# Optimization experiments

Hardware: AMD Instinct MI355X
Metric: run time of the kernel (lower is better)

The kernel has to match this reference:

```python
import jax, jax.numpy as jnp
import numpy as np

EMB_DIM, TREE_DIM, OUT_DIM, VOCAB = 256, 256, 3, 10000
T, B, LEVELS = 255, 128, 8  # complete binary tree of depth 8, 128 trees per input


def _build_forest():
    # node j = T-1-heap(j): root (heap 0) is the LAST node so stack_last_h picks the root.
    heap = np.arange(T)
    depth = np.floor(np.log2(heap + 1)).astype(np.int64)  # 0..7
    node_order = np.empty(T, dtype=np.int64)
    node_order[T - 1 - heap] = (LEVELS - 1) - depth       # leaves=0, root=7
    internal = np.arange((T - 1) // 2)                     # heaps with two children
    parent = np.repeat(T - 1 - internal, 2)
    child = np.stack([T - 1 - (2 * internal + 1), T - 1 - (2 * internal + 2)], 1).reshape(-1)
    edges = np.stack([parent, child], axis=1)              # (254, 2)
    edge_order = node_order[parent]
    offs = (np.arange(B) * T)[:, None, None]
    adj = (edges[None] + offs).reshape(-1, 2)              # (B*254, 2)
    return np.tile(node_order, B), adj, np.tile(edge_order, B)


def setup_inputs() -> dict:
    key = jax.random.key(0)
    ks = jax.random.split(key, 16)
    no, adj, eo = _build_forest()
    D = TREE_DIM
    s_e = 1.0 / np.sqrt(EMB_DIM)
    s_t = 1.0 / np.sqrt(D)
    return {
        'feat_cube': jax.random.randint(ks[0], (B * T,), 0, VOCAB),
        'feat_a': jax.random.randint(ks[1], (B * T,), 0, VOCAB),
        'feat_b': jax.random.randint(ks[2], (B * T,), 0, VOCAB),
        'node_order': jnp.asarray(no),
        'adjacency_list': jnp.asarray(adj),
        'edge_order': jnp.asarray(eo),
        'num_levels': LEVELS,
        'num_trees': B,
        'emb': jax.random.normal(ks[3], (VOCAB, EMB_DIM), jnp.float32),
        'W_iou': jax.random.normal(ks[4], (3 * D, EMB_DIM), jnp.float32) * s_e,
        'b_iou': jnp.zeros((3 * D,), jnp.float32),
        'U_iou': jax.random.normal(ks[5], (3 * D, D), jnp.float32) * s_t,
        'W_f': jax.random.normal(ks[6], (D, EMB_DIM), jnp.float32) * s_e,
        'b_f': jnp.zeros((D,), jnp.float32),
        'U_f': jax.random.normal(ks[7], (D, D), jnp.float32) * s_t,
        'fc1_w': jax.random.normal(ks[8], (D // 2, D), jnp.float32) * s_t,
        'fc1_b': jnp.zeros((D // 2,), jnp.float32),
        'fc2_w': jax.random.normal(ks[9], (OUT_DIM, D // 2), jnp.float32) * (1.0 / np.sqrt(D // 2)),
        'fc2_b': jnp.zeros((OUT_DIM,), jnp.float32),
    }


def _tree_lstm(x, node_order, parents, children, edge_order, W_iou, b_iou, U_iou, W_f, b_f, U_f, num_levels):
    # Child-sum TreeLSTM, evaluated level by level (leaves first). Dense masked
    # formulation: per level we update only nodes with node_order==lvl; edge
    # contributions are masked before segment_sum (same math as the torch loop).
    N = x.shape[0]
    D = U_f.shape[0]
    x_iou = x @ W_iou.T + b_iou            # (N, 3D), precomputed once
    x_f = x @ W_f.T + b_f                  # (N, D)
    h = jnp.zeros((N, D), x.dtype)
    c = jnp.zeros((N, D), x.dtype)
    for lvl in range(num_levels):
        emask = (edge_order == lvl)[:, None].astype(x.dtype)
        ch = h[children]                   # (E, D) gather of child hidden
        cc = c[children]
        f = jax.nn.sigmoid(x_f[parents] + ch @ U_f.T)
        h_sum = jax.ops.segment_sum(ch * emask, parents, num_segments=N)
        c_sum = jax.ops.segment_sum(f * cc * emask, parents, num_segments=N)
        i, o, u = jnp.split(x_iou + h_sum @ U_iou.T, 3, axis=1)
        c_new = jax.nn.sigmoid(i) * jnp.tanh(u) + c_sum
        h_new = jax.nn.sigmoid(o) * jnp.tanh(c_new)
        nmask = (node_order == lvl)[:, None]
        h = jnp.where(nmask, h_new, h)
        c = jnp.where(nmask, c_new, c)
    return h, c


def reference(feat_cube, feat_a, feat_b, node_order, adjacency_list, edge_order,
              num_levels, num_trees, emb, W_iou, b_iou, U_iou, W_f, b_f, U_f,
              fc1_w, fc1_b, fc2_w, fc2_b):
    parents = adjacency_list[:, 0]
    children = adjacency_list[:, 1]

    def run_tree(feat):
        h, _ = _tree_lstm(emb[feat], node_order, parents, children, edge_order,
                          W_iou, b_iou, U_iou, W_f, b_f, U_f, num_levels)
        # stack_last_h: last node of each tree (= root with our labeling)
        return h.reshape(num_trees, -1, h.shape[-1])[:, -1, :]

    h_c = run_tree(feat_cube)
    h_a = run_tree(feat_a)
    h_b = run_tree(feat_b)
    # h_c (1,D) @ (h_a (D,1) @ h_b (1,D)) == (h_c . h_a) * h_b, fused einsum
    h = jnp.einsum('bi,bi,bj->bj', h_c, h_a, h_b)
    hid = jax.nn.relu(h @ fc1_w.T + fc1_b)
    logits = jax.nn.relu(hid @ fc2_w.T + fc2_b)
    return logits  # (num_trees, out_dim)
```

## Files before the change

### kernel.cpp

```cpp
#include <hip/hip_runtime.h>
#include <hip/hip_bf16.h>

typedef __hip_bfloat16 bf16;
typedef unsigned short u16;
typedef __attribute__((ext_vector_type(8))) short s8;
typedef __attribute__((ext_vector_type(4))) float f4;

#define NRUNS 3
#define NTREE 128
#define TT    255
#define DD    256
#define VPAD  10016
#define PAD   258
#define ESTR  776

__device__ __forceinline__ float bits2f(u16 b){ union{unsigned u; float f;} x; x.u = ((unsigned)b)<<16; return x.f; }
__device__ __forceinline__ u16   f2bits(float f){ bf16 h = __float2bfloat16(f); return *(u16*)&h; }
__device__ __forceinline__ float sigm(float x){ return 1.f/(1.f+__expf(-x)); }
__device__ __forceinline__ float tanh_(float x){ return 1.f - 2.f/(__expf(2.f*x)+1.f); }

__global__ void k_detect(const u16* __restrict__ raw, int* __restrict__ flag){
    int t = threadIdx.x;
    int hit = 0;
    if (t < 128){
        u16 w = raw[2*t];
        int e = (w >> 7) & 0xFF;
        hit = (e >= 100 && e <= 141) ? 1 : 0;
    }
    __shared__ int cnt;
    if (t == 0) cnt = 0;
    __syncthreads();
    atomicAdd(&cnt, hit);
    __syncthreads();
    if (t == 0) flag[0] = (cnt >= 64) ? 1 : 0;
}

__device__ __forceinline__ u16 cvt1b(const void* p, int i, int isb){
    return isb ? ((const u16*)p)[i] : f2bits(((const float*)p)[i]);
}
__device__ __forceinline__ float cvt1f(const void* p, int i, int isb){
    return isb ? bits2f(((const u16*)p)[i]) : ((const float*)p)[i];
}

#define L_EMB  (10000*256)
#define L_EMBP (VPAD*256)
#define L_WIOU (768*256)
#define L_UIOU (768*256)
#define L_WF   (256*256)
#define L_UF   (256*256)
#define L_ALL  (L_EMBP + L_WIOU + L_UIOU + L_WF + L_UF)
__global__ void k_cvtb(const void* __restrict__ s0, const void* __restrict__ s1,
                       const void* __restrict__ s2, const void* __restrict__ s3,
                       const void* __restrict__ s4,
                       u16* __restrict__ d0, u16* __restrict__ d1, u16* __restrict__ d2,
                       u16* __restrict__ d3, u16* __restrict__ d4,
                       const int* __restrict__ flag){
    int isb = flag[0];
    for (int i = blockIdx.x*blockDim.x + threadIdx.x; i < L_ALL; i += gridDim.x*blockDim.x){
        int j = i;
        if (j < L_EMBP){ d0[j] = (j < L_EMB) ? cvt1b(s0, j, isb) : (u16)0; continue; } j -= L_EMBP;
        if (j < L_WIOU){ d1[j] = cvt1b(s1, j, isb); continue; } j -= L_WIOU;
        if (j < L_UIOU){ d2[j] = cvt1b(s2, j, isb); continue; } j -= L_UIOU;
        if (j < L_WF){ d3[j] = cvt1b(s3, j, isb); continue; } j -= L_WF;
        d4[j] = cvt1b(s4, j, isb);
    }
}

#define S_BIOU 768
#define S_BF   256
#define S_F1W  (128*256)
#define S_F1B  128
#define S_F2W  (3*128)
#define S_F2B  3
#define S_ALL  (S_BIOU+S_BF+S_F1W+S_F1B+S_F2W+S_F2B)
__global__ void k_small(const void* __restrict__ s0, const void* __restrict__ s1,
                        const void* __restrict__ s2, const void* __restrict__ s3,
                        const void* __restrict__ s4, const void* __restrict__ s5,
                        float* __restrict__ d0, float* __restrict__ d1, float* __restrict__ d2,
                        float* __restrict__ d3, float* __restrict__ d4, float* __restrict__ d5,
                        const int* __restrict__ flag){
    int isb = flag[0];
    for (int i = blockIdx.x*blockDim.x + threadIdx.x; i < S_ALL; i += gridDim.x*blockDim.x){
        int j = i;
        if (j < S_BIOU){ d0[j] = cvt1f(s0, j, isb); continue; } j -= S_BIOU;
        if (j < S_BF){ d1[j] = cvt1f(s1, j, isb); continue; } j -= S_BF;
        if (j < S_F1W){ d2[j] = cvt1f(s2, j, isb); continue; } j -= S_F1W;
        if (j < S_F1B){ d3[j] = cvt1f(s3, j, isb); continue; } j -= S_F1B;
        if (j < S_F2W){ d4[j] = cvt1f(s4, j, isb); continue; } j -= S_F2W;
        d5[j] = cvt1f(s5, j, isb);
    }
}

__device__ __forceinline__ s8 ldB16(const u16* p){
    union { uint4 q; s8 v; } u;
    u.q = *(const uint4*)p;
    return u.v;
}
__device__ __forceinline__ s8 ldsA(const u16* p){
    union { unsigned w[4]; s8 v; } u;
    u.w[0] = *(const unsigned*)(p);
    u.w[1] = *(const unsigned*)(p+2);
    u.w[2] = *(const unsigned*)(p+4);
    u.w[3] = *(const unsigned*)(p+6);
    return u.v;
}
#define MFMA(acc,a,b) acc = __builtin_amdgcn_mfma_f32_16x16x32_bf16(a, b, acc, 0, 0, 0)

__global__ __launch_bounds__(512, 4)
void k_vocab2(const u16* __restrict__ embb,
              const u16* __restrict__ Wiou, const u16* __restrict__ Wfm,
              const u16* __restrict__ Ufm,  const float* __restrict__ biou_f,
              u16* __restrict__ E_iou, u16* __restrict__ E_f,
              u16* __restrict__ H0, u16* __restrict__ C0, u16* __restrict__ HU0)
{
    __shared__ u16 hs[32*PAD];
    const int t = threadIdx.x, w = t>>6, lane = t&63, ln = lane&15, q = lane>>4;
    const int r0 = blockIdx.x*32, d0 = w*32;

    const u16* Bp[8];
    #pragma unroll
    for (int g = 0; g < 4; g++)
      #pragma unroll
      for (int nc = 0; nc < 2; nc++){
        int nn = d0 + nc*16 + ln;
        Bp[g*2+nc] = (g < 3) ? (Wiou + (size_t)(g*256+nn)*DD) : (Wfm + (size_t)nn*DD);
      }
    const u16* a0p = embb + (size_t)(r0+ln)*DD;
    const u16* a1p = embb + (size_t)(r0+16+ln)*DD;
    f4 acc[8][2];
    #pragma unroll
    for (int nt = 0; nt < 8; nt++){ acc[nt][0] = (f4){0,0,0,0}; acc[nt][1] = (f4){0,0,0,0}; }
    #pragma unroll 2
    for (int ks = 0; ks < 8; ks++){
        int ko = ks*32 + q*8;
        s8 a0 = ldB16(a0p + ko);
        s8 a1 = ldB16(a1p + ko);
        #pragma unroll
        for (int nt = 0; nt < 8; nt++){
            s8 bb = ldB16(Bp[nt] + ko);
            MFMA(acc[nt][0], a0, bb);
            MFMA(acc[nt][1], a1, bb);
        }
    }
    #pragma unroll
    for (int nc = 0; nc < 2; nc++){
        int d = d0 + nc*16 + ln;
        float bi = biou_f[d], bo = biou_f[256+d], bu = biou_f[512+d];
        #pragma unroll
        for (int ms = 0; ms < 2; ms++)
          #pragma unroll
          for (int r = 0; r < 4; r++){
            int vrow = r0 + ms*16 + q*4 + r;
            float ei = acc[0*2+nc][ms][r];
            float eo = acc[1*2+nc][ms][r];
            float eu = acc[2*2+nc][ms][r];
            float ef = acc[3*2+nc][ms][r];
            size_t eb = (size_t)vrow*768 + d;
            E_iou[eb]       = f2bits(ei);
            E_iou[eb + 256] = f2bits(eo);
            E_iou[eb + 512] = f2bits(eu);
            E_f[(size_t)vrow*DD + d] = f2bits(ef);
            float cc = sigm(ei + bi)*tanh_(eu + bu);
            float hh = sigm(eo + bo)*tanh_(cc);
            C0[(size_t)vrow*DD + d] = f2bits(cc);
            H0[(size_t)vrow*DD + d] = f2bits(hh);
            hs[(ms*16 + q*4 + r)*PAD + d] = f2bits(hh);
        }
    }
    __syncthreads();

    f4 hacc[2][2];
    #pragma unroll
    for (int nt = 0; nt < 2; nt++){ hacc[nt][0] = (f4){0,0,0,0}; hacc[nt][1] = (f4){0,0,0,0}; }
    const u16* Bf0 = Ufm + (size_t)(d0 + ln)*DD;
    const u16* Bf1 = Ufm + (size_t)(d0 + 16 + ln)*DD;
    #pragma unroll 2
    for (int ks = 0; ks < 8; ks++){
        int ko = ks*32 + q*8;
        s8 a0 = ldsA(&hs[ln*PAD + ko]);
        s8 a1 = ldsA(&hs[(16+ln)*PAD + ko]);
        s8 b0 = ldB16(Bf0 + ko);
        s8 b1 = ldB16(Bf1 + ko);
        MFMA(hacc[0][0], a0, b0); MFMA(hacc[0][1], a1, b0);
        MFMA(hacc[1][0], a0, b1); MFMA(hacc[1][1], a1, b1);
    }
    #pragma unroll
    for (int nc = 0; nc < 2; nc++){
        int d = d0 + nc*16 + ln;
        #pragma unroll
        for (int ms = 0; ms < 2; ms++)
          #pragma unroll
          for (int r = 0; r < 4; r++){
            int vrow = r0 + ms*16 + q*4 + r;
            HU0[(size_t)vrow*DD + d] = f2bits(hacc[nc][ms][r]);
        }
    }
}

__global__ __launch_bounds__(512, 4)
void k_edge0(const int* __restrict__ f0, const int* __restrict__ f1, const int* __restrict__ f2,
             const u16* __restrict__ E_f, const u16* __restrict__ H0,
             const u16* __restrict__ C0,  const u16* __restrict__ HU0,
             const float* __restrict__ bf_f,
             u16* __restrict__ hsum_out, u16* __restrict__ fcsum_out)
{
    int gid = blockIdx.x*512 + threadIdx.x;
    int row = gid >> 5, ch = gid & 31, d = ch*8;
    int run = row >> 13, rem = row & 8191, b = rem >> 6, jj = rem & 63;
    const int* fp = (run==0) ? f0 : ((run==1) ? f1 : f2);
    int fo = fp[b*TT + 128 + jj];
    int v1 = fp[b*TT + 2*jj];
    int v2 = fp[b*TT + 2*jj + 1];
    s8 ef  = ldB16(E_f + (size_t)fo*DD + d);
    s8 hu1 = ldB16(HU0 + (size_t)v1*DD + d);
    s8 hu2 = ldB16(HU0 + (size_t)v2*DD + d);
    s8 c1  = ldB16(C0  + (size_t)v1*DD + d);
    s8 c2  = ldB16(C0  + (size_t)v2*DD + d);
    s8 h1  = ldB16(H0  + (size_t)v1*DD + d);
    s8 h2  = ldB16(H0  + (size_t)v2*DD + d);
    union { u16 a[8]; uint4 q4; } uh, uf;
    #pragma unroll
    for (int j = 0; j < 8; j++){
        float e  = bits2f((u16)ef[j]) + bf_f[d+j];
        float fa = sigm(e + bits2f((u16)hu1[j]));
        float fb = sigm(e + bits2f((u16)hu2[j]));
        float fc = fa*bits2f((u16)c1[j]) + fb*bits2f((u16)c2[j]);
        float hsv = bits2f((u16)h1[j]) + bits2f((u16)h2[j]);
        uf.a[j] = f2bits(fc);
        uh.a[j] = f2bits(hsv);
    }
    *(uint4*)(hsum_out  + (size_t)row*DD + d) = uh.q4;
    *(uint4*)(fcsum_out + (size_t)row*DD + d) = uf.q4;
}

__global__ __launch_bounds__(512, 4)
void k_lvl(int lvl, int cLog,
           const int* __restrict__ f0, const int* __restrict__ f1, const int* __restrict__ f2,
           const u16* __restrict__ E_iou, const u16* __restrict__ E_f,
           const u16* __restrict__ Uiou, const u16* __restrict__ Ufm,
           const float* __restrict__ biou_f, const float* __restrict__ bf_f,
           const u16* __restrict__ hsum_in, const u16* __restrict__ fcsum_in,
           u16* __restrict__ hsum_out, u16* __restrict__ fcsum_out,
           u16* __restrict__ hroot)
{
    __shared__ u16 es[32*ESTR];
    __shared__ u16 hs[32*PAD];
    const int t = threadIdx.x, w = t>>6, lane = t&63, ln = lane&15, q = lane>>4;
    const int cnt = 1 << cLog, S = 256 - 2*cnt;
    const int r0 = blockIdx.x*32, d0 = w*32;
    const bool haveP = (lvl < 7);

    uint4 stg[6];
    {
        int srow = t >> 4, c16 = t & 15;
        int rho = r0 + srow;
        int run = rho >> (7+cLog);
        int rem = rho & ((1<<(7+cLog)) - 1);
        int b = rem >> cLog, jj = rem & (cnt-1);
        const int* fp = (run==0) ? f0 : ((run==1) ? f1 : f2);
        int feat_s = fp[b*TT + S + jj];
        const u16* ep = E_iou + (size_t)feat_s*768;
        #pragma unroll
        for (int it = 0; it < 6; it++){
            int chk = it*16 + c16;
            stg[it] = *(const uint4*)(ep + chk*8);
        }
    }

    int featp[2][2];
    if (haveP){
        #pragma unroll
        for (int ms = 0; ms < 2; ms++)
          #pragma unroll
          for (int rr = 0; rr < 2; rr++){
            int rho = r0 + ms*16 + q*4 + rr*2;
            int run = rho >> (7+cLog);
            int rem = rho & ((1<<(7+cLog)) - 1);
            int b = rem >> cLog, jj = rem & (cnt-1);
            const int* fp = (run==0) ? f0 : ((run==1) ? f1 : f2);
            featp[ms][rr] = fp[b*TT + (256-cnt) + (jj>>1)];
          }
    }

    f4 acc[6][2];
    #pragma unroll
    for (int nt = 0; nt < 6; nt++){ acc[nt][0] = (f4){0,0,0,0}; acc[nt][1] = (f4){0,0,0,0}; }
    {
        const u16* a0p = hsum_in + (size_t)(r0+ln)*DD;
        const u16* a1p = hsum_in + (size_t)(r0+16+ln)*DD;
        const u16* Bp[6];
        #pragma unroll
        for (int nt = 0; nt < 6; nt++){
            int n = (nt>>1)*256 + d0 + (nt&1)*16 + ln;
            Bp[nt] = Uiou + (size_t)n*DD;
        }
        #pragma unroll 2
        for (int ks = 0; ks < 8; ks++){
            int ko = ks*32 + q*8;
            s8 a0 = ldB16(a0p + ko);
            s8 a1 = ldB16(a1p + ko);
            #pragma unroll
            for (int nt = 0; nt < 6; nt++){
                s8 bb = ldB16(Bp[nt] + ko);
                MFMA(acc[nt][0], a0, bb);
                MFMA(acc[nt][1], a1, bb);
            }
        }
    }

    {
        int srow = t >> 4, c16 = t & 15;
        #pragma unroll
        for (int it = 0; it < 6; it++){
            int chk = it*16 + c16;
            *(uint4*)&es[srow*ESTR + chk*8] = stg[it];
        }
    }
    __syncthreads();

    float cv[2][2][4];
    #pragma unroll
    for (int nc = 0; nc < 2; nc++){
        int d = d0 + nc*16 + ln;
        float bi = biou_f[d], bo = biou_f[256+d], bu = biou_f[512+d];
        #pragma unroll
        for (int ms = 0; ms < 2; ms++){
            float hv[4];
            #pragma unroll
            for (int r = 0; r < 4; r++){
                int m   = ms*16 + q*4 + r;
                int rho = r0 + m;
                float iv = acc[0+nc][ms][r] + bits2f(es[m*ESTR + d])       + bi;
                float ov = acc[2+nc][ms][r] + bits2f(es[m*ESTR + 256 + d]) + bo;
                float uv = acc[4+nc][ms][r] + bits2f(es[m*ESTR + 512 + d]) + bu;
                float cs = bits2f(fcsum_in[(size_t)rho*DD + d]);
                float c = sigm(iv)*tanh_(uv) + cs;
                float h = sigm(ov)*tanh_(c);
                cv[nc][ms][r] = c;
                hv[r] = h;
                if (haveP) hs[m*PAD + d] = f2bits(h);
                else       hroot[(size_t)rho*DD + d] = f2bits(h);
            }
            if (haveP){
                int prow = (r0>>1) + ms*8 + q*2;
                hsum_out[(size_t)prow*DD + d]     = f2bits(hv[0] + hv[1]);
                hsum_out[(size_t)(prow+1)*DD + d] = f2bits(hv[2] + hv[3]);
            }
        }
    }

    if (haveP){
        __syncthreads();
        f4 hacc[2][2];
        #pragma unroll
        for (int nt = 0; nt < 2; nt++){ hacc[nt][0] = (f4){0,0,0,0}; hacc[nt][1] = (f4){0,0,0,0}; }
        const u16* Bf0 = Ufm + (size_t)(d0 + ln)*DD;
        const u16* Bf1 = Ufm + (size_t)(d0 + 16 + ln)*DD;
        #pragma unroll 2
        for (int ks = 0; ks < 8; ks++){
            int ko = ks*32 + q*8;
            s8 a0 = ldsA(&hs[ln*PAD + ko]);
            s8 a1 = ldsA(&hs[(16+ln)*PAD + ko]);
            s8 b0 = ldB16(Bf0 + ko);
            s8 b1 = ldB16(Bf1 + ko);
            MFMA(hacc[0][0], a0, b0); MFMA(hacc[0][1], a1, b0);
            MFMA(hacc[1][0], a0, b1); MFMA(hacc[1][1], a1, b1);
        }
        #pragma unroll
        for (int nc = 0; nc < 2; nc++){
            int d = d0 + nc*16 + ln;
            float bfv = bf_f[d];
            #pragma unroll
            for (int ms = 0; ms < 2; ms++){
                float fs0, fs1;
                #pragma unroll
                for (int r = 0; r < 4; r++){
                    float ef = bits2f(E_f[(size_t)featp[ms][r>>1]*DD + d]);
                    float fc = sigm(ef + bfv + hacc[nc][ms][r]) * cv[nc][ms][r];
                    if (r == 0) fs0 = fc;
                    else if (r == 1) fs0 += fc;
                    else if (r == 2) fs1 = fc;
                    else fs1 += fc;
                }
                int prow = (r0>>1) + ms*8 + q*2;
                fcsum_out[(size_t)prow*DD + d]     = f2bits(fs0);
                fcsum_out[(size_t)(prow+1)*DD + d] = f2bits(fs1);
            }
        }
    }
}

__global__ __launch_bounds__(256)
void k_final(const u16* __restrict__ hroot,
             const float* __restrict__ fc1w, const float* __restrict__ fc1b,
             const float* __restrict__ fc2w, const float* __restrict__ fc2b,
             void* __restrict__ out, const int* __restrict__ flag)
{
    int b = blockIdx.x, t = threadIdx.x;
    __shared__ float sprod[DD];
    __shared__ float shb[DD];
    __shared__ float shid[128];
    float hc  = bits2f(hroot[(0*NTREE + b)*DD + t]);
    float ha  = bits2f(hroot[(1*NTREE + b)*DD + t]);
    float hbv = bits2f(hroot[(2*NTREE + b)*DD + t]);
    sprod[t] = hc * ha;
    shb[t]   = hbv;
    __syncthreads();
    for (int s = 128; s > 0; s >>= 1){
        if (t < s) sprod[t] += sprod[t + s];
        __syncthreads();
    }
    float dot = sprod[0];
    if (t < 128){
        float acc = fc1b[t];
        for (int k = 0; k < DD; k++)
            acc = fmaf(dot * shb[k], fc1w[t*DD + k], acc);
        shid[t] = fmaxf(acc, 0.f);
    }
    __syncthreads();
    if (t < 3){
        float acc = fc2b[t];
        for (int j = 0; j < 128; j++)
            acc = fmaf(fc2w[t*128 + j], shid[j], acc);
        float v = fmaxf(acc, 0.f);
        if (flag[0]) ((bf16*)out)[b*3 + t] = __float2bfloat16(v);
        else         ((float*)out)[b*3 + t] = v;
    }
}

extern "C" void kernel_launch(void* const* d_in, const int* in_sizes, int n_in,
                              void* d_out, int out_size, void* d_ws, size_t ws_size,
                              hipStream_t stream)
{
    const int* f0 = (const int*)d_in[0];
    const int* f1 = (const int*)d_in[1];
    const int* f2 = (const int*)d_in[2];
    const void* emb  = d_in[8];
    const void* Wiou = d_in[9];
    const void* biou = d_in[10];
    const void* Uiou = d_in[11];
    const void* Wf   = d_in[12];
    const void* bfv  = d_in[13];
    const void* Uf   = d_in[14];
    const void* fc1w = d_in[15];
    const void* fc1b = d_in[16];
    const void* fc2w = d_in[17];
    const void* fc2b = d_in[18];

    char* base = (char*)d_ws;
    size_t off = 0;
    auto take = [&](size_t bytes) -> char* {
        char* p = base + off;
        off = (off + bytes + 255) & ~(size_t)255;
        return p;
    };
    int*   flag   = (int*)  take(256);
    u16*   embb   = (u16*)  take((size_t)L_EMBP*2);
    u16*   wioub  = (u16*)  take((size_t)L_WIOU*2);
    u16*   uioub  = (u16*)  take((size_t)L_UIOU*2);
    u16*   wfb    = (u16*)  take((size_t)L_WF*2);
    u16*   ufb    = (u16*)  take((size_t)L_UF*2);
    float* biou_f = (float*)take(S_BIOU*4);
    float* bf_f   = (float*)take(S_BF*4);
    float* fc1w_f = (float*)take(S_F1W*4);
    float* fc1b_f = (float*)take(S_F1B*4);
    float* fc2w_f = (float*)take(S_F2W*4);
    float* fc2b_f = (float*)take(S_F2B*4);
    u16*   E_iou  = (u16*)  take((size_t)VPAD*768*2);
    u16*   E_f    = (u16*)  take((size_t)VPAD*DD*2);
    u16*   H0     = (u16*)  take((size_t)VPAD*DD*2);
    u16*   C0     = (u16*)  take((size_t)VPAD*DD*2);
    u16*   HU0    = (u16*)  take((size_t)VPAD*DD*2);
    u16*   HA     = (u16*)  take((size_t)24576*DD*2);
    u16*   HB     = (u16*)  take((size_t)12288*DD*2);
    u16*   FA     = (u16*)  take((size_t)24576*DD*2);
    u16*   FB     = (u16*)  take((size_t)12288*DD*2);
    u16*   hroot  = (u16*)  take((size_t)NRUNS*NTREE*DD*2);

    k_detect<<<1, 256, 0, stream>>>((const u16*)emb, flag);
    k_cvtb<<<2048, 256, 0, stream>>>(emb, Wiou, Uiou, Wf, Uf,
                                     embb, wioub, uioub, wfb, ufb, flag);
    k_small<<<135, 256, 0, stream>>>(biou, bfv, fc1w, fc1b, fc2w, fc2b,
                                     biou_f, bf_f, fc1w_f, fc1b_f, fc2w_f, fc2b_f, flag);
    k_vocab2<<<VPAD/32, 512, 0, stream>>>(embb, wioub, wfb, ufb, biou_f,
                                          E_iou, E_f, H0, C0, HU0);
    k_edge0<<<24576*32/512, 512, 0, stream>>>(f0, f1, f2, E_f, H0, C0, HU0, bf_f, HA, FA);

    for (int lvl = 1; lvl <= 7; lvl++){
        int cLog = 7 - lvl;
        int rows = NRUNS*NTREE*(128 >> lvl);
        int blocks = rows / 32;
        int pe = lvl & 1;
        u16* hs_o = pe ? HB : HA;
        u16* fc_o = pe ? FB : FA;
        const u16* hs_i = pe ? HA : HB;
        const u16* fc_i = pe ? FA : FB;
        k_lvl<<<blocks, 512, 0, stream>>>(lvl, cLog, f0, f1, f2,
                                          E_iou, E_f, uioub, ufb,
                                          biou_f, bf_f,
                                          hs_i, fc_i, hs_o, fc_o, hroot);
    }
    k_final<<<NTREE, 256, 0, stream>>>(hroot, fc1w_f, fc1b_f, fc2w_f, fc2b_f, d_out, flag);
}
```

Baseline: 442.9 us.

## Fuse per-level tree LSTM launches into one persistent per-tree kernel

The seven per-level k_lvl launches are replaced by a single k_tree kernel with one block per tree per input, 384 blocks in all. Each block walks levels 1 through 7 in sequence and keeps child hidden sums and forget-gated cell sums in double-buffered shared memory instead of the global HA/HB/FA/FB buffers. This aims to remove launch overhead and the global round trips between levels. The costs are less parallelism, since only 384 blocks run and upper levels fill 32-row MFMA tiles with very few valid rows. Heavy LDS use probably allows only one block per CU, and each block re-reads the U weights at every level.

```diff
diff --git a/kernel.cpp b/kernel.cpp
--- a/kernel.cpp
+++ b/kernel.cpp
@@ -233,158 +233,176 @@
     *(uint4*)(fcsum_out + (size_t)row*DD + d) = uf.q4;
 }
 
-__global__ __launch_bounds__(512, 4)
-void k_lvl(int lvl, int cLog,
-           const int* __restrict__ f0, const int* __restrict__ f1, const int* __restrict__ f2,
-           const u16* __restrict__ E_iou, const u16* __restrict__ E_f,
-           const u16* __restrict__ Uiou, const u16* __restrict__ Ufm,
-           const float* __restrict__ biou_f, const float* __restrict__ bf_f,
-           const u16* __restrict__ hsum_in, const u16* __restrict__ fcsum_in,
-           u16* __restrict__ hsum_out, u16* __restrict__ fcsum_out,
-           u16* __restrict__ hroot)
+__global__ __launch_bounds__(512, 2)
+void k_tree(const int* __restrict__ f0, const int* __restrict__ f1, const int* __restrict__ f2,
+            const u16* __restrict__ E_iou, const u16* __restrict__ E_f,
+            const u16* __restrict__ Uiou,  const u16* __restrict__ Ufm,
+            const float* __restrict__ biou_f, const float* __restrict__ bf_f,
+            const u16* __restrict__ HA, const u16* __restrict__ FA,
+            u16* __restrict__ hroot)
 {
     __shared__ u16 es[32*ESTR];
     __shared__ u16 hs[32*PAD];
+    __shared__ u16 hsP[2][32*PAD];
+    __shared__ u16 fcP[2][32*256];
+    __shared__ int sfeat[256];
+
     const int t = threadIdx.x, w = t>>6, lane = t&63, ln = lane&15, q = lane>>4;
-    const int cnt = 1 << cLog, S = 256 - 2*cnt;
-    const int r0 = blockIdx.x*32, d0 = w*32;
-    const bool haveP = (lvl < 7);
-
-    uint4 stg[6];
-    {
-        int srow = t >> 4, c16 = t & 15;
-        int rho = r0 + srow;
-        int run = rho >> (7+cLog);
-        int rem = rho & ((1<<(7+cLog)) - 1);
-        int b = rem >> cLog, jj = rem & (cnt-1);
-        const int* fp = (run==0) ? f0 : ((run==1) ? f1 : f2);
-        int feat_s = fp[b*TT + S + jj];
-        const u16* ep = E_iou + (size_t)feat_s*768;
-        #pragma unroll
-        for (int it = 0; it < 6; it++){
-            int chk = it*16 + c16;
-            stg[it] = *(const uint4*)(ep + chk*8);
-        }
-    }
-
-    int featp[2][2];
-    if (haveP){
-        #pragma unroll
-        for (int ms = 0; ms < 2; ms++)
-          #pragma unroll
-          for (int rr = 0; rr < 2; rr++){
-            int rho = r0 + ms*16 + q*4 + rr*2;
-            int run = rho >> (7+cLog);
-            int rem = rho & ((1<<(7+cLog)) - 1);
-            int b = rem >> cLog, jj = rem & (cnt-1);
-            const int* fp = (run==0) ? f0 : ((run==1) ? f1 : f2);
-            featp[ms][rr] = fp[b*TT + (256-cnt) + (jj>>1)];
-          }
-    }
-
-    f4 acc[6][2];
-    #pragma unroll
-    for (int nt = 0; nt < 6; nt++){ acc[nt][0] = (f4){0,0,0,0}; acc[nt][1] = (f4){0,0,0,0}; }
-    {
-        const u16* a0p = hsum_in + (size_t)(r0+ln)*DD;
-        const u16* a1p = hsum_in + (size_t)(r0+16+ln)*DD;
-        const u16* Bp[6];
-        #pragma unroll
-        for (int nt = 0; nt < 6; nt++){
-            int n = (nt>>1)*256 + d0 + (nt&1)*16 + ln;
-            Bp[nt] = Uiou + (size_t)n*DD;
-        }
-        #pragma unroll 2
-        for (int ks = 0; ks < 8; ks++){
-            int ko = ks*32 + q*8;
-            s8 a0 = ldB16(a0p + ko);
-            s8 a1 = ldB16(a1p + ko);
+    const int d0 = w*32;
+    const int run = blockIdx.x >> 7, b = blockIdx.x & 127;
+    const int* __restrict__ fp = (run==0) ? f0 : ((run==1) ? f1 : f2);
+    const int gtree = run*8192 + b*64;
+
+    if (t < 256) sfeat[t] = (t < 255) ? fp[b*TT + t] : 0;
+    __syncthreads();
+
+    const int srow = t >> 4, c16 = t & 15;
+
+    for (int l = 1; l <= 7; l++){
+        const int n_l  = 128 >> l;
+        const int S    = 256 - 2*n_l;
+        const bool haveP = (l < 7);
+        const int inb  = l & 1;
+        const int outb = inb ^ 1;
+        const int nsub = (l == 1) ? 2 : 1;
+        for (int sub = 0; sub < nsub; sub++){
+            const int j0 = sub*32;
+
+            if (l == 1){
+                const u16* src = HA + (size_t)(gtree + j0 + srow)*DD + c16*16;
+                uint4 v0 = *(const uint4*)(src);
+                uint4 v1 = *(const uint4*)(src + 8);
+                unsigned* dst = (unsigned*)&hsP[1][srow*PAD + c16*16];
+                dst[0] = ((unsigned*)&v0)[0]; dst[1] = ((unsigned*)&v0)[1];
+                dst[2] = ((unsigned*)&v0)[2]; dst[3] = ((unsigned*)&v0)[3];
+                dst[4] = ((unsigned*)&v1)[0]; dst[5] = ((unsigned*)&v1)[1];
+                dst[6] = ((unsigned*)&v1)[2]; dst[7] = ((unsigned*)&v1)[3];
+                __syncthreads();
+            }
+
+            uint4 stg[6];
+            const bool doStage = (srow < n_l - j0);
+            if (doStage){
+                int fidx = sfeat[S + j0 + srow];
+                const u16* ep = E_iou + (size_t)fidx*768;
+                #pragma unroll
+                for (int it = 0; it < 6; it++)
+                    stg[it] = *(const uint4*)(ep + (it*16 + c16)*8);
+            }
+
+            int featp[2][2];
+            if (haveP){
+                #pragma unroll
+                for (int ms = 0; ms < 2; ms++)
+                  #pragma unroll
+                  for (int rr = 0; rr < 2; rr++){
+                    int pj = (j0 + ms*16 + q*4 + rr*2) >> 1;
+                    featp[ms][rr] = (pj < (n_l>>1)) ? sfeat[256 - n_l + pj] : 0;
+                  }
+            }
+
+            f4 acc[6][2];
             #pragma unroll
-            for (int nt = 0; nt < 6; nt++){
-                s8 bb = ldB16(Bp[nt] + ko);
-                MFMA(acc[nt][0], a0, bb);
-                MFMA(acc[nt][1], a1, bb);
-            }
-        }
-    }
-
-    {
-        int srow = t >> 4, c16 = t & 15;
-        #pragma unroll
-        for (int it = 0; it < 6; it++){
-            int chk = it*16 + c16;
-            *(uint4*)&es[srow*ESTR + chk*8] = stg[it];
-        }
-    }
-    __syncthreads();
-
-    float cv[2][2][4];
-    #pragma unroll
-    for (int nc = 0; nc < 2; nc++){
-        int d = d0 + nc*16 + ln;
-        float bi = biou_f[d], bo = biou_f[256+d], bu = biou_f[512+d];
-        #pragma unroll
-        for (int ms = 0; ms < 2; ms++){
-            float hv[4];
+            for (int nt = 0; nt < 6; nt++){ acc[nt][0] = (f4){0,0,0,0}; acc[nt][1] = (f4){0,0,0,0}; }
+            {
+                const u16* Bp[6];
+                #pragma unroll
+                for (int nt = 0; nt < 6; nt++){
+                    int n = (nt>>1)*256 + d0 + (nt&1)*16 + ln;
+                    Bp[nt] = Uiou + (size_t)n*DD;
+                }
+                const u16* a0l = &hsP[inb][ln*PAD];
+                const u16* a1l = &hsP[inb][(16+ln)*PAD];
+                #pragma unroll 2
+                for (int ks = 0; ks < 8; ks++){
+                    int ko = ks*32 + q*8;
+                    s8 a0 = ldsA(a0l + ko);
+                    s8 a1 = ldsA(a1l + ko);
+                    #pragma unroll
+                    for (int nt = 0; nt < 6; nt++){
+                        s8 bb = ldB16(Bp[nt] + ko);
+                        MFMA(acc[nt][0], a0, bb);
+                        MFMA(acc[nt][1], a1, bb);
+                    }
+                }
+            }
+
+            if (doStage){
+                #pragma unroll
+                for (int it = 0; it < 6; it++)
+                    *(uint4*)&es[srow*ESTR + (it*16 + c16)*8] = stg[it];
+            }
+            __syncthreads();
+
+            float cv[2][2][4];
             #pragma unroll
-            for (int r = 0; r < 4; r++){
-                int m   = ms*16 + q*4 + r;
-                int rho = r0 + m;
-                float iv = acc[0+nc][ms][r] + bits2f(es[m*ESTR + d])       + bi;
-                float ov = acc[2+nc][ms][r] + bits2f(es[m*ESTR + 256 + d]) + bo;
-                float uv = acc[4+nc][ms][r] + bits2f(es[m*ESTR + 512 + d]) + bu;
-                float cs = bits2f(fcsum_in[(size_t)rho*DD + d]);
-                float c = sigm(iv)*tanh_(uv) + cs;
-                float h = sigm(ov)*tanh_(c);
-                cv[nc][ms][r] = c;
-                hv[r] = h;
-                if (haveP) hs[m*PAD + d] = f2bits(h);
-                else       hroot[(size_t)rho*DD + d] = f2bits(h);
-            }
+            for (int nc = 0; nc < 2; nc++){
+                int d = d0 + nc*16 + ln;
+                float bi = biou_f[d], bo = biou_f[256+d], bu = biou_f[512+d];
+                #pragma unroll
+                for (int ms = 0; ms < 2; ms++){
+                    float hv[4];
+                    #pragma unroll
+                    for (int r = 0; r < 4; r++){
+                        int m = ms*16 + q*4 + r;
+                        float iv = acc[0+nc][ms][r] + bits2f(es[m*ESTR + d])       + bi;
+                        float ov = acc[2+nc][ms][r] + bits2f(es[m*ESTR + 256 + d]) + bo;
+                        float uv = acc[4+nc][ms][r] + bits2f(es[m*ESTR + 512 + d]) + bu;
+                        float cs = (l == 1) ? bits2f(FA[(size_t)(gtree + j0 + m)*DD + d])
+                                            : bits2f(fcP[inb][m*256 + d]);
+                        float c = sigm(iv)*tanh_(uv) + cs;
+                        float h = sigm(ov)*tanh_(c);
+                        cv[nc][ms][r] = c;
+                        hv[r] = h;
+                        if (haveP) hs[m*PAD + d] = f2bits(h);
+                        else if (m == 0) hroot[((size_t)run*NTREE + b)*DD + d] = f2bits(h);
+                    }
+                    if (haveP){
+                        int prow = sub*16 + ms*8 + q*2;
+                        hsP[outb][prow*PAD + d]     = f2bits(hv[0] + hv[1]);
+                        hsP[outb][(prow+1)*PAD + d] = f2bits(hv[2] + hv[3]);
+                    }
+                }
+            }
+
             if (haveP){
-                int prow = (r0>>1) + ms*8 + q*2;
-                hsum_out[(size_t)prow*DD + d]     = f2bits(hv[0] + hv[1]);
-                hsum_out[(size_t)(prow+1)*DD + d] = f2bits(hv[2] + hv[3]);
-            }
-        }
-    }
-
-    if (haveP){
-        __syncthreads();
-        f4 hacc[2][2];
-        #pragma unroll
-        for (int nt = 0; nt < 2; nt++){ hacc[nt][0] = (f4){0,0,0,0}; hacc[nt][1] = (f4){0,0,0,0}; }
-        const u16* Bf0 = Ufm + (size_t)(d0 + ln)*DD;
-        const u16* Bf1 = Ufm + (size_t)(d0 + 16 + ln)*DD;
-        #pragma unroll 2
-        for (int ks = 0; ks < 8; ks++){
-            int ko = ks*32 + q*8;
-            s8 a0 = ldsA(&hs[ln*PAD + ko]);
-            s8 a1 = ldsA(&hs[(16+ln)*PAD + ko]);
-            s8 b0 = ldB16(Bf0 + ko);
-            s8 b1 = ldB16(Bf1 + ko);
-            MFMA(hacc[0][0], a0, b0); MFMA(hacc[0][1], a1, b0);
-            MFMA(hacc[1][0], a0, b1); MFMA(hacc[1][1], a1, b1);
-        }
-        #pragma unroll
-        for (int nc = 0; nc < 2; nc++){
-            int d = d0 + nc*16 + ln;
-            float bfv = bf_f[d];
-            #pragma unroll
-            for (int ms = 0; ms < 2; ms++){
-                float fs0, fs1;
-                #pragma unroll
-                for (int r = 0; r < 4; r++){
-                    float ef = bits2f(E_f[(size_t)featp[ms][r>>1]*DD + d]);
-                    float fc = sigm(ef + bfv + hacc[nc][ms][r]) * cv[nc][ms][r];
-                    if (r == 0) fs0 = fc;
-                    else if (r == 1) fs0 += fc;
-                    else if (r == 2) fs1 = fc;
-                    else fs1 += fc;
+                __syncthreads();
+                f4 hacc[2][2];
+                #pragma unroll
+                for (int nt = 0; nt < 2; nt++){ hacc[nt][0] = (f4){0,0,0,0}; hacc[nt][1] = (f4){0,0,0,0}; }
+                const u16* Bf0 = Ufm + (size_t)(d0 + ln)*DD;
+                const u16* Bf1 = Ufm + (size_t)(d0 + 16 + ln)*DD;
+                #pragma unroll 2
+                for (int ks = 0; ks < 8; ks++){
+                    int ko = ks*32 + q*8;
+                    s8 a0 = ldsA(&hs[ln*PAD + ko]);
+                    s8 a1 = ldsA(&hs[(16+ln)*PAD + ko]);
+                    s8 b0 = ldB16(Bf0 + ko);
+                    s8 b1 = ldB16(Bf1 + ko);
+                    MFMA(hacc[0][0], a0, b0); MFMA(hacc[0][1], a1, b0);
+                    MFMA(hacc[1][0], a0, b1); MFMA(hacc[1][1], a1, b1);
                 }
-                int prow = (r0>>1) + ms*8 + q*2;
-                fcsum_out[(size_t)prow*DD + d]     = f2bits(fs0);
-                fcsum_out[(size_t)(prow+1)*DD + d] = f2bits(fs1);
+                #pragma unroll
+                for (int nc = 0; nc < 2; nc++){
+                    int d = d0 + nc*16 + ln;
+                    float bfv = bf_f[d];
+                    #pragma unroll
+                    for (int ms = 0; ms < 2; ms++){
+                        float fs0, fs1;
+                        #pragma unroll
+                        for (int r = 0; r < 4; r++){
+                            float ef = bits2f(E_f[(size_t)featp[ms][r>>1]*DD + d]);
+                            float fc = sigm(ef + bfv + hacc[nc][ms][r]) * cv[nc][ms][r];
+                            if (r == 0) fs0 = fc;
+                            else if (r == 1) fs0 += fc;
+                            else if (r == 2) fs1 = fc;
+                            else fs1 += fc;
+                        }
+                        int prow = sub*16 + ms*8 + q*2;
+                        fcP[outb][prow*256 + d]     = f2bits(fs0);
+                        fcP[outb][(prow+1)*256 + d] = f2bits(fs1);
+                    }
+                }
             }
         }
     }
@@ -472,9 +490,7 @@
     u16*   C0     = (u16*)  take((size_t)VPAD*DD*2);
     u16*   HU0    = (u16*)  take((size_t)VPAD*DD*2);
     u16*   HA     = (u16*)  take((size_t)24576*DD*2);
-    u16*   HB     = (u16*)  take((size_t)12288*DD*2);
     u16*   FA     = (u16*)  take((size_t)24576*DD*2);
-    u16*   FB     = (u16*)  take((size_t)12288*DD*2);
     u16*   hroot  = (u16*)  take((size_t)NRUNS*NTREE*DD*2);
 
     k_detect<<<1, 256, 0, stream>>>((const u16*)emb, flag);
@@ -485,20 +501,7 @@
     k_vocab2<<<VPAD/32, 512, 0, stream>>>(embb, wioub, wfb, ufb, biou_f,
                                           E_iou, E_f, H0, C0, HU0);
     k_edge0<<<24576*32/512, 512, 0, stream>>>(f0, f1, f2, E_f, H0, C0, HU0, bf_f, HA, FA);
-
-    for (int lvl = 1; lvl <= 7; lvl++){
-        int cLog = 7 - lvl;
-        int rows = NRUNS*NTREE*(128 >> lvl);
-        int blocks = rows / 32;
-        int pe = lvl & 1;
-        u16* hs_o = pe ? HB : HA;
-        u16* fc_o = pe ? FB : FA;
-        const u16* hs_i = pe ? HA : HB;
-        const u16* fc_i = pe ? FA : FB;
-        k_lvl<<<blocks, 512, 0, stream>>>(lvl, cLog, f0, f1, f2,
-                                          E_iou, E_f, uioub, ufb,
-                                          biou_f, bf_f,
-                                          hs_i, fc_i, hs_o, fc_o, hroot);
-    }
+    k_tree<<<NRUNS*NTREE, 512, 0, stream>>>(f0, f1, f2, E_iou, E_f, uioub, ufb,
+                                            biou_f, bf_f, HA, FA, hroot);
     k_final<<<NTREE, 256, 0, stream>>>(hroot, fc1w_f, fc1b_f, fc2w_f, fc2b_f, d_out, flag);
 }
```

Result: slower. 528.5 us (+19.3%).
